# Kernel tuning notes

Hardware: AMD Instinct MI355X
Metric: run time of the kernel (lower is better)

The kernel has to match this reference:

```python
import jax, jax.numpy as jnp
import numpy as np

N_EMBD = 1024
N_HEAD = 16
HEAD_DIM = N_EMBD // N_HEAD
B, T, I = 8, 1024, 257


def _ln(x, g, b, eps=1e-5):
    mu = jnp.mean(x, axis=-1, keepdims=True)
    var = jnp.var(x, axis=-1, keepdims=True)
    return (x - mu) * jax.lax.rsqrt(var + eps) * g + b


def setup_inputs() -> dict:
    key = jax.random.key(0)
    ks = jax.random.split(key, 16)
    s = 0.02
    d = {
        "x": jax.random.normal(ks[0], (B, T, N_EMBD), jnp.float32),
        "encoder_output": jax.random.normal(ks[1], (B, I, N_EMBD), jnp.float32),
        # LayerNorm params
        "ln1_g": jnp.ones((N_EMBD,), jnp.float32), "ln1_b": jnp.zeros((N_EMBD,), jnp.float32),
        "ln2_g": jnp.ones((N_EMBD,), jnp.float32), "ln2_b": jnp.zeros((N_EMBD,), jnp.float32),
        "ln3_g": jnp.ones((N_EMBD,), jnp.float32), "ln3_b": jnp.zeros((N_EMBD,), jnp.float32),
        # self-attention
        "w_qkv": jax.random.normal(ks[2], (N_EMBD, 3 * N_EMBD), jnp.float32) * s,
        "b_qkv": jnp.zeros((3 * N_EMBD,), jnp.float32),
        "w_ao": jax.random.normal(ks[3], (N_EMBD, N_EMBD), jnp.float32) * s,
        "b_ao": jnp.zeros((N_EMBD,), jnp.float32),
        # cross-attention
        "w_q": jax.random.normal(ks[4], (N_EMBD, N_EMBD), jnp.float32) * s,
        "b_q": jnp.zeros((N_EMBD,), jnp.float32),
        "w_kv": jax.random.normal(ks[5], (N_EMBD, 2 * N_EMBD), jnp.float32) * s,
        "b_kv": jnp.zeros((2 * N_EMBD,), jnp.float32),
        "w_co": jax.random.normal(ks[6], (N_EMBD, N_EMBD), jnp.float32) * s,
        "b_co": jnp.zeros((N_EMBD,), jnp.float32),
        # MLP
        "w_fc": jax.random.normal(ks[7], (N_EMBD, 4 * N_EMBD), jnp.float32) * s,
        "b_fc": jnp.zeros((4 * N_EMBD,), jnp.float32),
        "w_mo": jax.random.normal(ks[8], (4 * N_EMBD, N_EMBD), jnp.float32) * s,
        "b_mo": jnp.zeros((N_EMBD,), jnp.float32),
    }
    return d


def _heads(t, L):
    # [B, L, C] -> [B, H, L, D]
    return t.reshape(B, L, N_HEAD, HEAD_DIM).transpose(0, 2, 1, 3)


def _self_attn(x, w_qkv, b_qkv, w_ao, b_ao):
    qkv = x @ w_qkv + b_qkv
    q, k, v = jnp.split(qkv, 3, axis=-1)
    q, k, v = _heads(q, T), _heads(k, T), _heads(v, T)
    att = jnp.einsum('bhtd,bhsd->bhts', q, k) * (1.0 / np.sqrt(HEAD_DIM))
    causal = jnp.tril(jnp.ones((T, T), bool))
    att = jnp.where(causal, att, -jnp.inf)
    att = jax.nn.softmax(att, axis=-1)
    out = jnp.einsum('bhts,bhsd->bhtd', att, v).transpose(0, 2, 1, 3).reshape(B, T, N_EMBD)
    return out @ w_ao + b_ao


def _cross_attn(x, enc, w_q, b_q, w_kv, b_kv, w_co, b_co):
    q = _heads(x @ w_q + b_q, T)
    kv = enc @ w_kv + b_kv
    k, v = jnp.split(kv, 2, axis=-1)
    k, v = _heads(k, I), _heads(v, I)
    att = jnp.einsum('bhtd,bhid->bhti', q, k) * (1.0 / np.sqrt(HEAD_DIM))
    att = jax.nn.softmax(att, axis=-1)
    out = jnp.einsum('bhti,bhid->bhtd', att, v).transpose(0, 2, 1, 3).reshape(B, T, N_EMBD)
    return out @ w_co + b_co


def reference(x, encoder_output, ln1_g, ln1_b, ln2_g, ln2_b, ln3_g, ln3_b,
              w_qkv, b_qkv, w_ao, b_ao, w_q, b_q, w_kv, b_kv, w_co, b_co,
              w_fc, b_fc, w_mo, b_mo):
    x = x + _self_attn(_ln(x, ln1_g, ln1_b), w_qkv, b_qkv, w_ao, b_ao)
    x = x + _cross_attn(_ln(x, ln2_g, ln2_b), encoder_output, w_q, b_q, w_kv, b_kv, w_co, b_co)
    h = _ln(x, ln3_g, ln3_b)
    h = jax.nn.gelu(h @ w_fc + b_fc, approximate=True)  # GELU tanh approximation
    x = x + h @ w_mo + b_mo
    return x
```

## Files before the change

### kernel.cpp

```cpp
#include <hip/hip_runtime.h>
#include <hip/hip_bf16.h>

#define N_EMBD 1024
#define N_HEAD 16
#define HEAD_DIM 64
#define BATCH 8
#define SEQ_T 1024
#define SEQ_I 257

typedef __attribute__((ext_vector_type(8))) short short8_t;
typedef __attribute__((ext_vector_type(4))) float f32x4;

union U8 { uint4 u; short8_t s; };

static __device__ __forceinline__ unsigned short f2b(float f)
{
    unsigned int u = __float_as_uint(f);
    u = (u + 0x7fffu + ((u >> 16) & 1u)) >> 16;
    return (unsigned short)u;
}
static __device__ __forceinline__ float b2f_lo(unsigned int u) { return __uint_as_float(u << 16); }
static __device__ __forceinline__ float b2f_hi(unsigned int u) { return __uint_as_float(u & 0xffff0000u); }

__device__ __forceinline__ float gelu_tanh(float u)
{
    float z = 0.7978845608028654f * (u + 0.044715f * u * u * u);
    z = fmaxf(z, -15.0f);
    const float e = __expf(-2.0f * z);
    const float t = (1.0f - e) / (1.0f + e);
    return 0.5f * u * (1.0f + t);
}

__global__ __launch_bounds__(256)
void wcast_t(const float* __restrict__ W, short* __restrict__ WT, int K, int N)
{
    __shared__ float t[32][33];
    const int n0 = blockIdx.x * 32, k0 = blockIdx.y * 32;
    const int c = threadIdx.x & 31, r4 = (threadIdx.x >> 5) * 4;
    #pragma unroll
    for (int i = 0; i < 4; ++i)
        t[r4 + i][c] = W[(size_t)(k0 + r4 + i) * N + n0 + c];
    __syncthreads();
    #pragma unroll
    for (int i = 0; i < 4; ++i)
        WT[(size_t)(n0 + r4 + i) * K + k0 + c] = (short)f2b(t[c][r4 + i]);
}

__global__ __launch_bounds__(256)
void cast_bf16(const float* __restrict__ in, short* __restrict__ out)
{
    const int i = blockIdx.x * 256 + threadIdx.x;
    const float4 v = ((const float4*)in)[i];
    unsigned int w0 = (unsigned int)f2b(v.x) | ((unsigned int)f2b(v.y) << 16);
    unsigned int w1 = (unsigned int)f2b(v.z) | ((unsigned int)f2b(v.w) << 16);
    ((uint2*)out)[i] = make_uint2(w0, w1);
}

__global__ __launch_bounds__(256)
void ln_bf16(const float* __restrict__ in, const float* __restrict__ gamma,
             const float* __restrict__ beta, short* __restrict__ out)
{
    const int row = blockIdx.x;
    const int tid = threadIdx.x;
    const float4 v = *(const float4*)(in + (size_t)row * N_EMBD + tid * 4);
    float s  = v.x + v.y + v.z + v.w;
    float ss = v.x*v.x + v.y*v.y + v.z*v.z + v.w*v.w;
    #pragma unroll
    for (int off = 32; off >= 1; off >>= 1) {
        s  += __shfl_down(s,  off);
        ss += __shfl_down(ss, off);
    }
    __shared__ float rs[4], rss[4];
    const int wid = tid >> 6, lane = tid & 63;
    if (lane == 0) { rs[wid] = s; rss[wid] = ss; }
    __syncthreads();
    s  = rs[0] + rs[1] + rs[2] + rs[3];
    ss = rss[0] + rss[1] + rss[2] + rss[3];
    const float mean = s * (1.0f / N_EMBD);
    const float var  = ss * (1.0f / N_EMBD) - mean * mean;
    const float rstd = rsqrtf(var + 1e-5f);
    const float4 g = *(const float4*)(gamma + tid * 4);
    const float4 b = *(const float4*)(beta  + tid * 4);
    float o0 = (v.x - mean) * rstd * g.x + b.x;
    float o1 = (v.y - mean) * rstd * g.y + b.y;
    float o2 = (v.z - mean) * rstd * g.z + b.z;
    float o3 = (v.w - mean) * rstd * g.w + b.w;
    unsigned int w0 = (unsigned int)f2b(o0) | ((unsigned int)f2b(o1) << 16);
    unsigned int w1 = (unsigned int)f2b(o2) | ((unsigned int)f2b(o3) << 16);
    ((uint2*)(out + (size_t)row * N_EMBD))[tid] = make_uint2(w0, w1);
}

template<int EPI>
__global__ __launch_bounds__(256, 2)
void gemm_mfma(const short* __restrict__ A, const short* __restrict__ WT,
               const float* __restrict__ bias, const float* __restrict__ res,
               void* __restrict__ outv, int M, int N, int K, int lda)
{
    __shared__ short As[128 * 32];
    __shared__ short Bs[128 * 32];
    const int tid  = threadIdx.x;
    const int bm   = blockIdx.y * 128;
    const int bn   = blockIdx.x * 128;
    const int lane = tid & 63;
    const int wid  = tid >> 6;
    const int wr   = (wid >> 1) * 64;
    const int wc   = (wid & 1) * 64;
    const int fr   = lane & 15;
    const int kg   = lane >> 4;

    const int idx0 = tid;
    const int idx1 = 256 + tid;
    const int r0 = idx0 >> 2, g0 = (idx0 & 3) ^ ((r0 >> 1) & 3);
    const int r1 = idx1 >> 2, g1 = (idx1 & 3) ^ ((r1 >> 1) & 3);
    const short* aSrc0 = A  + (size_t)min(bm + r0, M - 1) * lda + g0 * 8;
    const short* aSrc1 = A  + (size_t)min(bm + r1, M - 1) * lda + g1 * 8;
    const short* bSrc0 = WT + (size_t)(bn + r0) * K + g0 * 8;
    const short* bSrc1 = WT + (size_t)(bn + r1) * K + g1 * 8;
    const int dst0 = (tid & ~63) * 16;
    const int dst1 = (256 + (tid & ~63)) * 16;

    int offA[4], offB[4];
    #pragma unroll
    for (int f = 0; f < 4; ++f) {
        const int ra = wr + f * 16 + fr;
        offA[f] = ra * 32 + ((kg ^ ((ra >> 1) & 3)) * 8);
        const int rb = wc + f * 16 + fr;
        offB[f] = rb * 32 + ((kg ^ ((rb >> 1) & 3)) * 8);
    }

    f32x4 acc[4][4];
    #pragma unroll
    for (int i = 0; i < 4; ++i)
        #pragma unroll
        for (int j = 0; j < 4; ++j)
            acc[i][j] = (f32x4){0.f, 0.f, 0.f, 0.f};

    for (int k0 = 0; k0 < K; k0 += 32) {
        __builtin_amdgcn_global_load_lds(
            (const __attribute__((address_space(1))) void*)(aSrc0 + k0),
            (__attribute__((address_space(3))) void*)((char*)As + dst0), 16, 0, 0);
        __builtin_amdgcn_global_load_lds(
            (const __attribute__((address_space(1))) void*)(aSrc1 + k0),
            (__attribute__((address_space(3))) void*)((char*)As + dst1), 16, 0, 0);
        __builtin_amdgcn_global_load_lds(
            (const __attribute__((address_space(1))) void*)(bSrc0 + k0),
            (__attribute__((address_space(3))) void*)((char*)Bs + dst0), 16, 0, 0);
        __builtin_amdgcn_global_load_lds(
            (const __attribute__((address_space(1))) void*)(bSrc1 + k0),
            (__attribute__((address_space(3))) void*)((char*)Bs + dst1), 16, 0, 0);
        __syncthreads();
        short8_t af[4], bf[4];
        #pragma unroll
        for (int f = 0; f < 4; ++f) {
            af[f] = *(const short8_t*)(As + offA[f]);
            bf[f] = *(const short8_t*)(Bs + offB[f]);
        }
        #pragma unroll
        for (int i = 0; i < 4; ++i)
            #pragma unroll
            for (int j = 0; j < 4; ++j)
                acc[i][j] = __builtin_amdgcn_mfma_f32_16x16x32_bf16(af[i], bf[j], acc[i][j], 0, 0, 0);
        __syncthreads();
    }

    #pragma unroll
    for (int i = 0; i < 4; ++i) {
        #pragma unroll
        for (int r = 0; r < 4; ++r) {
            const int m = bm + wr + i * 16 + kg * 4 + r;
            if (m >= M) continue;
            #pragma unroll
            for (int j = 0; j < 4; ++j) {
                const int n = bn + wc + j * 16 + fr;
                float v = acc[i][j][r] + bias[n];
                if (EPI == 1) v += res[(size_t)m * N + n];
                if (EPI == 2) v = gelu_tanh(v);
                if (EPI == 1) ((float*)outv)[(size_t)m * N + n] = v;
                else          ((short*)outv)[(size_t)m * N + n] = (short)f2b(v);
            }
        }
    }
}

template<bool CAUSAL>
__global__ __launch_bounds__(256, 2)
void attn_mfma(const short* __restrict__ Qm, const short* __restrict__ Km,
               const short* __restrict__ Vm, short* __restrict__ out,
               int qStride, int kStride, int kRows)
{
    __shared__ short Ks[32 * 64];
    __shared__ unsigned int VtU[36 * 32];
    __shared__ unsigned int PA[4][320];

    const int tid  = threadIdx.x;
    const int lane = tid & 63;
    const int wid  = tid >> 6;
    const int bid  = blockIdx.x;
    const int qt   = CAUSAL ? (15 - (bid >> 7)) : (bid >> 7);
    const int bh   = bid & 127;
    const int b    = bh >> 4, h = bh & 15;
    const int qb   = qt * 64;
    const int fr   = lane & 15;
    const int g    = lane >> 4;

    const int qrow = qb + wid * 16 + fr;
    const short* qptr = Qm + (size_t)(b * SEQ_T + qrow) * qStride + h * HEAD_DIM + g * 8;
    U8 qf0, qf1;
    qf0.u = *(const uint4*)(qptr);
    qf1.u = *(const uint4*)(qptr + 32);

    f32x4 accO[4];
    #pragma unroll
    for (int i = 0; i < 4; ++i) accO[i] = (f32x4){0.f, 0.f, 0.f, 0.f};
    float mrun = -1e30f, lrun = 0.f;

    const int ntiles = CAUSAL ? (2 * qt + 2) : ((kRows + 31) >> 5);
    const size_t kbase = (size_t)b * kRows;

    for (int it = 0; it < ntiles; ++it) {
        const int kb = it * 32;
        __syncthreads();

        {
            const int krow  = min(kb + (tid >> 3), kRows - 1);
            const int gslot = (tid & 7) ^ ((tid >> 3) & 7);
            __builtin_amdgcn_global_load_lds(
                (const __attribute__((address_space(1))) void*)
                    (Km + (kbase + krow) * (size_t)kStride + h * HEAD_DIM + gslot * 8),
                (__attribute__((address_space(3))) void*)((char*)Ks + tid * 16), 16, 0, 0);
        }
        #pragma unroll
        for (int v = 0; v < 2; ++v) {
            const int idx = v * 256 + tid;
            const int d2 = idx & 31, kp = idx >> 5;
            const int kr0 = min(kb + 2 * kp,     kRows - 1);
            const int kr1 = min(kb + 2 * kp + 1, kRows - 1);
            const unsigned int u0 = *(const unsigned int*)
                (Vm + (kbase + kr0) * (size_t)kStride + h * HEAD_DIM + 2 * d2);
            const unsigned int u1 = *(const unsigned int*)
                (Vm + (kbase + kr1) * (size_t)kStride + h * HEAD_DIM + 2 * d2);
            VtU[36 * d2 + kp]      = (u0 & 0xffffu) | (u1 << 16);
            VtU[36 * d2 + 18 + kp] = (u0 >> 16)    | (u1 & 0xffff0000u);
        }
        __syncthreads();

        f32x4 s0 = (f32x4){0.f,0.f,0.f,0.f}, s1 = (f32x4){0.f,0.f,0.f,0.f};
        {
            const uint4* K4 = (const uint4*)Ks;
            U8 ka;
            ka.u = K4[8 * fr        + ((g)     ^ (fr & 7))];
            s0 = __builtin_amdgcn_mfma_f32_16x16x32_bf16(ka.s, qf0.s, s0, 0, 0, 0);
            ka.u = K4[8 * fr        + ((4 + g) ^ (fr & 7))];
            s0 = __builtin_amdgcn_mfma_f32_16x16x32_bf16(ka.s, qf1.s, s0, 0, 0, 0);
            ka.u = K4[8 * (16 + fr) + ((g)     ^ (fr & 7))];
            s1 = __builtin_amdgcn_mfma_f32_16x16x32_bf16(ka.s, qf0.s, s1, 0, 0, 0);
            ka.u = K4[8 * (16 + fr) + ((4 + g) ^ (fr & 7))];
            s1 = __builtin_amdgcn_mfma_f32_16x16x32_bf16(ka.s, qf1.s, s1, 0, 0, 0);
        }

        float sv[8];
        #pragma unroll
        for (int r = 0; r < 4; ++r) {
            sv[r]     = s0[r] * 0.125f;
            sv[4 + r] = s1[r] * 0.125f;
            const int k0 = kb + 4 * g + r;
            const int k1 = k0 + 16;
            if (CAUSAL ? (k0 > qrow) : (k0 >= kRows)) sv[r]     = -1e30f;
            if (CAUSAL ? (k1 > qrow) : (k1 >= kRows)) sv[4 + r] = -1e30f;
        }
        float tm = sv[0];
        #pragma unroll
        for (int j = 1; j < 8; ++j) tm = fmaxf(tm, sv[j]);
        tm = fmaxf(tm, __shfl_xor(tm, 16));
        tm = fmaxf(tm, __shfl_xor(tm, 32));
        const float newm = fmaxf(mrun, tm);
        const float fs = __expf(mrun - newm);
        mrun = newm;
        float p[8], ps = 0.f;
        #pragma unroll
        for (int j = 0; j < 8; ++j) { p[j] = __expf(sv[j] - newm); ps += p[j]; }
        ps += __shfl_xor(ps, 16);
        ps += __shfl_xor(ps, 32);
        lrun = lrun * fs + ps;

        float frr[4];
        #pragma unroll
        for (int r = 0; r < 4; ++r) frr[r] = __shfl(fs, 4 * g + r);
        #pragma unroll
        for (int db = 0; db < 4; ++db)
            #pragma unroll
            for (int r = 0; r < 4; ++r) accO[db][r] *= frr[r];

        {
            uint2* paw = (uint2*)PA[wid];
            paw[10 * fr + g] = make_uint2(
                (unsigned int)f2b(p[0]) | ((unsigned int)f2b(p[1]) << 16),
                (unsigned int)f2b(p[2]) | ((unsigned int)f2b(p[3]) << 16));
            paw[10 * fr + 4 + g] = make_uint2(
                (unsigned int)f2b(p[4]) | ((unsigned int)f2b(p[5]) << 16),
                (unsigned int)f2b(p[6]) | ((unsigned int)f2b(p[7]) << 16));
        }
        U8 pf;
        pf.u = ((const uint4*)PA[wid])[5 * fr + g];

        #pragma unroll
        for (int db = 0; db < 4; ++db) {
            const int d = db * 16 + fr;
            const uint2 v0 = ((const uint2*)VtU)[9 * d + 2 * g];
            const uint2 v1 = ((const uint2*)VtU)[9 * d + 2 * g + 1];
            U8 vf; vf.u = make_uint4(v0.x, v0.y, v1.x, v1.y);
            accO[db] = __builtin_amdgcn_mfma_f32_16x16x32_bf16(pf.s, vf.s, accO[db], 0, 0, 0);
        }
    }

    float lr[4];
    #pragma unroll
    for (int r = 0; r < 4; ++r) lr[r] = 1.0f / __shfl(lrun, 4 * g + r);
    #pragma unroll
    for (int db = 0; db < 4; ++db) {
        #pragma unroll
        for (int r = 0; r < 4; ++r) {
            const int row = qb + wid * 16 + 4 * g + r;
            const int col = h * HEAD_DIM + db * 16 + fr;
            out[(size_t)(b * SEQ_T + row) * N_EMBD + col] = (short)f2b(accO[db][r] * lr[r]);
        }
    }
}

extern "C" void kernel_launch(void* const* d_in, const int* in_sizes, int n_in,
                              void* d_out, int out_size, void* d_ws, size_t ws_size,
                              hipStream_t stream)
{
    const float* x     = (const float*)d_in[0];
    const float* enc   = (const float*)d_in[1];
    const float* ln1_g = (const float*)d_in[2];
    const float* ln1_b = (const float*)d_in[3];
    const float* ln2_g = (const float*)d_in[4];
    const float* ln2_b = (const float*)d_in[5];
    const float* ln3_g = (const float*)d_in[6];
    const float* ln3_b = (const float*)d_in[7];
    const float* w_qkv = (const float*)d_in[8];
    const float* b_qkv = (const float*)d_in[9];
    const float* w_ao  = (const float*)d_in[10];
    const float* b_ao  = (const float*)d_in[11];
    const float* w_q   = (const float*)d_in[12];
    const float* b_q   = (const float*)d_in[13];
    const float* w_kv  = (const float*)d_in[14];
    const float* b_kv  = (const float*)d_in[15];
    const float* w_co  = (const float*)d_in[16];
    const float* b_co  = (const float*)d_in[17];
    const float* w_fc  = (const float*)d_in[18];
    const float* b_fc  = (const float*)d_in[19];
    const float* w_mo  = (const float*)d_in[20];
    const float* b_mo  = (const float*)d_in[21];
    float* outp = (float*)d_out;

    short* wt_qkv = (short*)d_ws;
    short* wt_ao  = wt_qkv + 3145728;
    short* wt_q   = wt_ao  + 1048576;
    short* wt_kv  = wt_q   + 1048576;
    short* wt_co  = wt_kv  + 2097152;
    short* wt_fc  = wt_co  + 1048576;
    short* wt_mo  = wt_fc  + 4194304;
    short* enc_b  = wt_mo  + 4194304;
    short* y_b    = enc_b  + 2105344;
    short* qkv_b  = y_b    + 8388608;
    short* h_b    = qkv_b;
    short* attn_b = qkv_b  + 33554432;
    short* q_b    = attn_b + 8388608;
    float* x1     = (float*)(q_b + 8388608);
    float* x2     = x1 + 8388608;
    short* kv_b   = (short*)(x2 + 8388608);

    const int ROWS  = BATCH * SEQ_T;
    const int EROWS = BATCH * SEQ_I;

    wcast_t<<<dim3(3072/32, 1024/32), 256, 0, stream>>>(w_qkv, wt_qkv, 1024, 3072);
    wcast_t<<<dim3(1024/32, 1024/32), 256, 0, stream>>>(w_ao,  wt_ao,  1024, 1024);
    wcast_t<<<dim3(1024/32, 1024/32), 256, 0, stream>>>(w_q,   wt_q,   1024, 1024);
    wcast_t<<<dim3(2048/32, 1024/32), 256, 0, stream>>>(w_kv,  wt_kv,  1024, 2048);
    wcast_t<<<dim3(1024/32, 1024/32), 256, 0, stream>>>(w_co,  wt_co,  1024, 1024);
    wcast_t<<<dim3(4096/32, 1024/32), 256, 0, stream>>>(w_fc,  wt_fc,  1024, 4096);
    wcast_t<<<dim3(1024/32, 4096/32), 256, 0, stream>>>(w_mo,  wt_mo,  4096, 1024);
    cast_bf16<<<2056, 256, 0, stream>>>(enc, enc_b);

    ln_bf16<<<ROWS, 256, 0, stream>>>(x, ln1_g, ln1_b, y_b);
    gemm_mfma<0><<<dim3(3072/128, ROWS/128), 256, 0, stream>>>(
        y_b, wt_qkv, b_qkv, nullptr, qkv_b, ROWS, 3072, 1024, 1024);
    attn_mfma<true><<<2048, 256, 0, stream>>>(
        qkv_b, qkv_b + 1024, qkv_b + 2048, attn_b, 3072, 3072, SEQ_T);
    gemm_mfma<1><<<dim3(1024/128, ROWS/128), 256, 0, stream>>>(
        attn_b, wt_ao, b_ao, x, x1, ROWS, 1024, 1024, 1024);
    ln_bf16<<<ROWS, 256, 0, stream>>>(x1, ln2_g, ln2_b, y_b);
    gemm_mfma<0><<<dim3(1024/128, ROWS/128), 256, 0, stream>>>(
        y_b, wt_q, b_q, nullptr, q_b, ROWS, 1024, 1024, 1024);
    gemm_mfma<0><<<dim3(2048/128, (EROWS+127)/128), 256, 0, stream>>>(
        enc_b, wt_kv, b_kv, nullptr, kv_b, EROWS, 2048, 1024, 1024);
    attn_mfma<false><<<2048, 256, 0, stream>>>(
        q_b, kv_b, kv_b + 1024, attn_b, 1024, 2048, SEQ_I);
    gemm_mfma<1><<<dim3(1024/128, ROWS/128), 256, 0, stream>>>(
        attn_b, wt_co, b_co, x1, x2, ROWS, 1024, 1024, 1024);
    ln_bf16<<<ROWS, 256, 0, stream>>>(x2, ln3_g, ln3_b, y_b);
    gemm_mfma<2><<<dim3(4096/128, ROWS/128), 256, 0, stream>>>(
        y_b, wt_fc, b_fc, nullptr, h_b, ROWS, 4096, 1024, 1024);
    gemm_mfma<1><<<dim3(1024/128, ROWS/128), 256, 0, stream>>>(
        h_b, wt_mo, b_mo, x2, outp, ROWS, 1024, 4096, 4096);
}
```

Before: 708.8 us.

## Double-buffer GEMM LDS with 64-wide K tiles and XCD-aware block remap

The bf16 MFMA GEMM now loads 64-wide K tiles into two LDS buffers, issuing the next tile's global-to-LDS copies before computing on the current one. This halves the number of barriers per K and hides some load latency. The grid becomes 1D, with a remap that groups consecutive tiles onto the same XCD for better L2 reuse. LDS use per block grows fourfold, which may pressure occupancy.

```diff
diff --git a/kernel.cpp b/kernel.cpp
--- a/kernel.cpp
+++ b/kernel.cpp
@@ -19,8 +19,6 @@
     u = (u + 0x7fffu + ((u >> 16) & 1u)) >> 16;
     return (unsigned short)u;
 }
-static __device__ __forceinline__ float b2f_lo(unsigned int u) { return __uint_as_float(u << 16); }
-static __device__ __forceinline__ float b2f_hi(unsigned int u) { return __uint_as_float(u & 0xffff0000u); }
 
 __device__ __forceinline__ float gelu_tanh(float u)
 {
@@ -94,13 +92,17 @@
 __global__ __launch_bounds__(256, 2)
 void gemm_mfma(const short* __restrict__ A, const short* __restrict__ WT,
                const float* __restrict__ bias, const float* __restrict__ res,
-               void* __restrict__ outv, int M, int N, int K, int lda)
-{
-    __shared__ short As[128 * 32];
-    __shared__ short Bs[128 * 32];
+               void* __restrict__ outv, int M, int N, int K, int lda, int gnx)
+{
+    __shared__ short As[2][128 * 64];
+    __shared__ short Bs[2][128 * 64];
     const int tid  = threadIdx.x;
-    const int bm   = blockIdx.y * 128;
-    const int bn   = blockIdx.x * 128;
+
+    const int nwg = gridDim.x;
+    const int lin = (blockIdx.x & 7) * (nwg >> 3) + (blockIdx.x >> 3);
+    const int bm  = (lin / gnx) * 128;
+    const int bn  = (lin % gnx) * 128;
+
     const int lane = tid & 63;
     const int wid  = tid >> 6;
     const int wr   = (wid >> 1) * 64;
@@ -108,25 +110,26 @@
     const int fr   = lane & 15;
     const int kg   = lane >> 4;
 
-    const int idx0 = tid;
-    const int idx1 = 256 + tid;
-    const int r0 = idx0 >> 2, g0 = (idx0 & 3) ^ ((r0 >> 1) & 3);
-    const int r1 = idx1 >> 2, g1 = (idx1 & 3) ^ ((r1 >> 1) & 3);
-    const short* aSrc0 = A  + (size_t)min(bm + r0, M - 1) * lda + g0 * 8;
-    const short* aSrc1 = A  + (size_t)min(bm + r1, M - 1) * lda + g1 * 8;
-    const short* bSrc0 = WT + (size_t)(bn + r0) * K + g0 * 8;
-    const short* bSrc1 = WT + (size_t)(bn + r1) * K + g1 * 8;
-    const int dst0 = (tid & ~63) * 16;
-    const int dst1 = (256 + (tid & ~63)) * 16;
-
-    int offA[4], offB[4];
-    #pragma unroll
-    for (int f = 0; f < 4; ++f) {
-        const int ra = wr + f * 16 + fr;
-        offA[f] = ra * 32 + ((kg ^ ((ra >> 1) & 3)) * 8);
-        const int rb = wc + f * 16 + fr;
-        offB[f] = rb * 32 + ((kg ^ ((rb >> 1) & 3)) * 8);
-    }
+    const int r_ = tid >> 3;
+    const int g_ = (tid & 7) ^ (r_ & 7);
+    const int dstbase = (tid & ~63) * 16;
+
+    #define STAGE(buf, k0)                                                          \
+        _Pragma("unroll")                                                           \
+        for (int p = 0; p < 4; ++p) {                                               \
+            const int rowA = min(bm + p * 32 + r_, M - 1);                          \
+            __builtin_amdgcn_global_load_lds(                                       \
+                (const __attribute__((address_space(1))) void*)                     \
+                    (A + (size_t)rowA * lda + (k0) + g_ * 8),                       \
+                (__attribute__((address_space(3))) void*)                           \
+                    ((char*)As[buf] + p * 4096 + dstbase), 16, 0, 0);               \
+            const int rowB = bn + p * 32 + r_;                                      \
+            __builtin_amdgcn_global_load_lds(                                       \
+                (const __attribute__((address_space(1))) void*)                     \
+                    (WT + (size_t)rowB * K + (k0) + g_ * 8),                        \
+                (__attribute__((address_space(3))) void*)                           \
+                    ((char*)Bs[buf] + p * 4096 + dstbase), 16, 0, 0);               \
+        }
 
     f32x4 acc[4][4];
     #pragma unroll
@@ -135,33 +138,35 @@
         for (int j = 0; j < 4; ++j)
             acc[i][j] = (f32x4){0.f, 0.f, 0.f, 0.f};
 
-    for (int k0 = 0; k0 < K; k0 += 32) {
-        __builtin_amdgcn_global_load_lds(
-            (const __attribute__((address_space(1))) void*)(aSrc0 + k0),
-            (__attribute__((address_space(3))) void*)((char*)As + dst0), 16, 0, 0);
-        __builtin_amdgcn_global_load_lds(
-            (const __attribute__((address_space(1))) void*)(aSrc1 + k0),
-            (__attribute__((address_space(3))) void*)((char*)As + dst1), 16, 0, 0);
-        __builtin_amdgcn_global_load_lds(
-            (const __attribute__((address_space(1))) void*)(bSrc0 + k0),
-            (__attribute__((address_space(3))) void*)((char*)Bs + dst0), 16, 0, 0);
-        __builtin_amdgcn_global_load_lds(
-            (const __attribute__((address_space(1))) void*)(bSrc1 + k0),
-            (__attribute__((address_space(3))) void*)((char*)Bs + dst1), 16, 0, 0);
-        __syncthreads();
-        short8_t af[4], bf[4];
-        #pragma unroll
-        for (int f = 0; f < 4; ++f) {
-            af[f] = *(const short8_t*)(As + offA[f]);
-            bf[f] = *(const short8_t*)(Bs + offB[f]);
-        }
-        #pragma unroll
-        for (int i = 0; i < 4; ++i)
+    STAGE(0, 0);
+    __syncthreads();
+
+    const int nkt = K >> 6;
+    for (int kt = 0; kt < nkt; ++kt) {
+        const int cur = kt & 1;
+        if (kt + 1 < nkt) { STAGE(cur ^ 1, (kt + 1) << 6); }
+
+        const short* AsC = As[cur];
+        const short* BsC = Bs[cur];
+        #pragma unroll
+        for (int kk = 0; kk < 2; ++kk) {
+            short8_t af[4], bf[4];
             #pragma unroll
-            for (int j = 0; j < 4; ++j)
-                acc[i][j] = __builtin_amdgcn_mfma_f32_16x16x32_bf16(af[i], bf[j], acc[i][j], 0, 0, 0);
+            for (int f = 0; f < 4; ++f) {
+                const int ra = wr + f * 16 + fr;
+                af[f] = *(const short8_t*)(AsC + ra * 64 + (((kk * 4 + kg) ^ (ra & 7)) * 8));
+                const int rb = wc + f * 16 + fr;
+                bf[f] = *(const short8_t*)(BsC + rb * 64 + (((kk * 4 + kg) ^ (rb & 7)) * 8));
+            }
+            #pragma unroll
+            for (int i = 0; i < 4; ++i)
+                #pragma unroll
+                for (int j = 0; j < 4; ++j)
+                    acc[i][j] = __builtin_amdgcn_mfma_f32_16x16x32_bf16(af[i], bf[j], acc[i][j], 0, 0, 0);
+        }
         __syncthreads();
     }
+    #undef STAGE
 
     #pragma unroll
     for (int i = 0; i < 4; ++i) {
@@ -385,24 +390,24 @@
     cast_bf16<<<2056, 256, 0, stream>>>(enc, enc_b);
 
     ln_bf16<<<ROWS, 256, 0, stream>>>(x, ln1_g, ln1_b, y_b);
-    gemm_mfma<0><<<dim3(3072/128, ROWS/128), 256, 0, stream>>>(
-        y_b, wt_qkv, b_qkv, nullptr, qkv_b, ROWS, 3072, 1024, 1024);
+    gemm_mfma<0><<<1536, 256, 0, stream>>>(
+        y_b, wt_qkv, b_qkv, nullptr, qkv_b, ROWS, 3072, 1024, 1024, 24);
     attn_mfma<true><<<2048, 256, 0, stream>>>(
         qkv_b, qkv_b + 1024, qkv_b + 2048, attn_b, 3072, 3072, SEQ_T);
-    gemm_mfma<1><<<dim3(1024/128, ROWS/128), 256, 0, stream>>>(
-        attn_b, wt_ao, b_ao, x, x1, ROWS, 1024, 1024, 1024);
+    gemm_mfma<1><<<512, 256, 0, stream>>>(
+        attn_b, wt_ao, b_ao, x, x1, ROWS, 1024, 1024, 1024, 8);
     ln_bf16<<<ROWS, 256, 0, stream>>>(x1, ln2_g, ln2_b, y_b);
-    gemm_mfma<0><<<dim3(1024/128, ROWS/128), 256, 0, stream>>>(
-        y_b, wt_q, b_q, nullptr, q_b, ROWS, 1024, 1024, 1024);
-    gemm_mfma<0><<<dim3(2048/128, (EROWS+127)/128), 256, 0, stream>>>(
-        enc_b, wt_kv, b_kv, nullptr, kv_b, EROWS, 2048, 1024, 1024);
+    gemm_mfma<0><<<512, 256, 0, stream>>>(
+        y_b, wt_q, b_q, nullptr, q_b, ROWS, 1024, 1024, 1024, 8);
+    gemm_mfma<0><<<272, 256, 0, stream>>>(
+        enc_b, wt_kv, b_kv, nullptr, kv_b, EROWS, 2048, 1024, 1024, 16);
     attn_mfma<false><<<2048, 256, 0, stream>>>(
         q_b, kv_b, kv_b + 1024, attn_b, 1024, 2048, SEQ_I);
-    gemm_mfma<1><<<dim3(1024/128, ROWS/128), 256, 0, stream>>>(
-        attn_b, wt_co, b_co, x1, x2, ROWS, 1024, 1024, 1024);
+    gemm_mfma<1><<<512, 256, 0, stream>>>(
+        attn_b, wt_co, b_co, x1, x2, ROWS, 1024, 1024, 1024, 8);
     ln_bf16<<<ROWS, 256, 0, stream>>>(x2, ln3_g, ln3_b, y_b);
-    gemm_mfma<2><<<dim3(4096/128, ROWS/128), 256, 0, stream>>>(
-        y_b, wt_fc, b_fc, nullptr, h_b, ROWS, 4096, 1024, 1024);
-    gemm_mfma<1><<<dim3(1024/128, ROWS/128), 256, 0, stream>>>(
-        h_b, wt_mo, b_mo, x2, outp, ROWS, 1024, 4096, 4096);
-}
+    gemm_mfma<2><<<2048, 256, 0, stream>>>(
+        y_b, wt_fc, b_fc, nullptr, h_b, ROWS, 4096, 1024, 1024, 32);
+    gemm_mfma<1><<<512, 256, 0, stream>>>(
+        h_b, wt_mo, b_mo, x2, outp, ROWS, 1024, 4096, 4096, 8);
+}
```

Result: faster. 672.1 us (-5.2%).
